# Optimization experiments

Measured on AMD Instinct MI355X. Metric: run time of the kernel, lower is better.

The kernel has to match this reference:

```python
import jax, jax.numpy as jnp
import numpy as np

B, S, HID = 1, 2048, 2048
H = 16
DN, DR, DV = 128, 64, 128          # qk_nope_head_dim, qk_rope_head_dim, v_head_dim
DQ = DN + DR                        # q_head_dim = 192
QLR, KVLR = 1536, 512               # q_lora_rank, kv_lora_rank
MAXP = 32 * 1024
SCALE = DQ ** -0.5
EPS = 1e-6


def rmsnorm(x, w):
    return x * jax.lax.rsqrt(jnp.mean(x * x, axis=-1, keepdims=True) + EPS) * w


def rotate_half(x):
    h = x.shape[-1] // 2
    return jnp.concatenate((-x[..., h:], x[..., :h]), axis=-1)


def interleave_to_half(x):
    # torch: view(b,h,s,d//2,2).transpose(4,3).reshape(b,h,s,d)
    b, h, s, d = x.shape
    return x.reshape(b, h, s, d // 2, 2).transpose(0, 1, 2, 4, 3).reshape(b, h, s, d)


def setup_inputs() -> dict:
    key = jax.random.key(0)
    ks = jax.random.split(key, 8)
    def w(k, shape):
        fan_in = shape[-1]
        return jax.random.normal(k, shape, jnp.float32) * (fan_in ** -0.5)
    inp = {
        "hidden_states": jax.random.normal(ks[0], (B, S, HID), jnp.float32),
        "q_a_w": w(ks[1], (QLR, HID)),
        "q_a_ln": jnp.ones((QLR,), jnp.float32),
        "q_b_w": w(ks[2], (H * DQ, QLR)),
        "kv_a_w": w(ks[3], (KVLR + DR, HID)),
        "kv_a_ln": jnp.ones((KVLR,), jnp.float32),
        "kv_b_w": w(ks[4], (H * (DN + DV), KVLR)),
        "o_w": w(ks[5], (HID, H * DV)),
    }
    # rotary tables, seq_len = 32k
    inv_freq = 1.0 / (10000.0 ** (np.arange(0, DR, 2, dtype=np.float32) / DR))
    t = np.arange(MAXP, dtype=np.float32)
    freqs = np.outer(t, inv_freq)
    emb = np.concatenate((freqs, freqs), axis=-1)
    inp["cos"] = jnp.asarray(np.cos(emb), jnp.float32)
    inp["sin"] = jnp.asarray(np.sin(emb), jnp.float32)
    # bool mask, True = masked (causal)
    inp["attention_mask"] = jnp.triu(jnp.ones((S, S), bool), 1)[None, None]
    inp["position_ids"] = jnp.arange(S, dtype=jnp.int64 if jax.config.jax_enable_x64 else jnp.int32)[None].repeat(B, 0)
    return inp


def reference(hidden_states, q_a_w, q_a_ln, q_b_w, kv_a_w, kv_a_ln, kv_b_w, o_w,
              cos, sin, attention_mask, position_ids):
    b, s, _ = hidden_states.shape
    # low-rank Q: q_b(LN(q_a(x)))
    q = rmsnorm(hidden_states @ q_a_w.T, q_a_ln) @ q_b_w.T         # [b,s,H*DQ]
    q = q.reshape(b, s, H, DQ).transpose(0, 2, 1, 3)               # [b,H,s,DQ]
    q_nope, q_pe = q[..., :DN], q[..., DN:]
    # compressed KV + decoupled rope key
    ckv = hidden_states @ kv_a_w.T                                  # [b,s,KVLR+DR]
    compressed_kv, k_pe = ckv[..., :KVLR], ckv[..., KVLR:]
    k_pe = k_pe.reshape(b, s, 1, DR).transpose(0, 2, 1, 3)          # [b,1,s,DR]
    kv = rmsnorm(compressed_kv, kv_a_ln) @ kv_b_w.T                 # [b,s,H*(DN+DV)]
    kv = kv.reshape(b, s, H, DN + DV).transpose(0, 2, 1, 3)         # [b,H,s,DN+DV]
    k_nope, value_states = kv[..., :DN], kv[..., DN:]
    # rotary with interleaved->half reorder on the rope slice only
    cos_p = cos[position_ids][:, None]                              # [b,1,s,DR]
    sin_p = sin[position_ids][:, None]
    q_pe = interleave_to_half(q_pe)
    k_pe = interleave_to_half(k_pe)
    q_pe = q_pe * cos_p + rotate_half(q_pe) * sin_p
    k_pe = k_pe * cos_p + rotate_half(k_pe) * sin_p
    query_states = jnp.concatenate((q_nope, q_pe), axis=-1)         # [b,H,s,DQ]
    key_states = jnp.concatenate(
        (k_nope, jnp.broadcast_to(k_pe, (b, H, s, DR))), axis=-1)   # [b,H,s,DQ]
    # manual attention
    scores = jnp.einsum("bhqd,bhkd->bhqk", query_states, key_states) * SCALE
    scores = jnp.where(attention_mask, jnp.float32(-10000.0), scores)
    attn = jax.nn.softmax(scores.astype(jnp.float32), axis=-1).astype(query_states.dtype)
    attn_out = jnp.einsum("bhqk,bhkd->bhqd", attn, value_states)    # [b,H,s,DV]
    attn_out = attn_out.transpose(0, 2, 1, 3).reshape(b, s, H * DV)
    return attn_out @ o_w.T                                         # [b,s,HID]
```

## Files before the change

kernel.cpp:

```cpp
#include <hip/hip_runtime.h>
#include <stdint.h>

typedef unsigned short u16;
typedef __attribute__((ext_vector_type(8))) short short8;
typedef __attribute__((ext_vector_type(4))) float f32x4;
typedef __attribute__((ext_vector_type(4))) unsigned short ushort4_t;
typedef __attribute__((ext_vector_type(4))) float float4_t;

#define DEV_INLINE __device__ __forceinline__

DEV_INLINE u16 f2bf(float f) {
    union { float f; unsigned u; } x; x.f = f;
    unsigned u = x.u;
    unsigned r = (u + 0x7FFFu + ((u >> 16) & 1u)) >> 16;
    return (u16)r;
}

DEV_INLINE float bf2f(u16 b) {
    union { unsigned u; float f; } x; x.u = ((unsigned)b) << 16;
    return x.f;
}

DEV_INLINE float fexp2(float x) {
    float r;
    asm("v_exp_f32 %0, %1" : "=v"(r) : "v"(x));
    return r;
}

__global__ void conv_multi(const float* __restrict__ s0, u16* __restrict__ d0, long e0,
                           const float* __restrict__ s1, u16* __restrict__ d1, long e1,
                           const float* __restrict__ s2, u16* __restrict__ d2, long e2,
                           const float* __restrict__ s3, u16* __restrict__ d3, long e3,
                           const float* __restrict__ s4, u16* __restrict__ d4, long e4) {
    long i = (long)blockIdx.x * 256 + threadIdx.x;
    const float* s; u16* d; long base;
    if      (i < e0) { s = s0; d = d0; base = 0; }
    else if (i < e1) { s = s1; d = d1; base = e0; }
    else if (i < e2) { s = s2; d = d2; base = e1; }
    else if (i < e3) { s = s3; d = d3; base = e2; }
    else if (i < e4) { s = s4; d = d4; base = e3; }
    else return;
    long j = i - base;
    float4_t v = ((const float4_t*)s)[j];
    ushort4_t o;
    o.x = f2bf(v.x); o.y = f2bf(v.y); o.z = f2bf(v.z); o.w = f2bf(v.w);
    ((ushort4_t*)d)[j] = o;
}

__global__ void conv_pad(const float* __restrict__ in, u16* __restrict__ out,
                         int rows_valid, long n4, int cols4) {
    long i = (long)blockIdx.x * blockDim.x + threadIdx.x;
    if (i >= n4) return;
    long row = i / cols4;
    ushort4_t o; o.x = 0; o.y = 0; o.z = 0; o.w = 0;
    if (row < rows_valid) {
        float4_t v = ((const float4_t*)in)[i];
        o.x = f2bf(v.x); o.y = f2bf(v.y); o.z = f2bf(v.z); o.w = f2bf(v.w);
    }
    ((ushort4_t*)out)[i] = o;
}

#define BK 32

DEV_INLINE void gload16(const u16* g, u16* l) {
    __builtin_amdgcn_global_load_lds((const __attribute__((address_space(1))) unsigned int*)g,
                                     (__attribute__((address_space(3))) unsigned int*)l,
                                     16, 0, 0);
}

template <typename OT>
__global__ __launch_bounds__(256) void gemm64_db(const u16* __restrict__ A, const u16* __restrict__ B,
                                                 OT* __restrict__ C, int M, int N, int K) {
    __shared__ u16 As[2][64 * BK];
    __shared__ u16 Bs[2][128 * BK];
    const int tid = threadIdx.x;
    const int wid = tid >> 6, lane = tid & 63;
    const int lm = lane & 15, lk = lane >> 4;
    const long bm = (long)blockIdx.y * 64, bn = (long)blockIdx.x * 128;

    f32x4 acc[4][2] = {};

    const int rowS = lane >> 2;
    const int colS = ((lane & 3) ^ ((lane >> 3) & 3)) * 8;
    const int cs = (lm >> 1) & 3;
    const u16* Ag = A + (bm + wid * 16 + rowS) * (long)K + colS;
    const u16* Bg = B + (bn + wid * 32 + rowS) * (long)K + colS;
    const int aoff = wid * 16 * BK;
    const int boff = wid * 32 * BK;

    gload16(Ag, &As[0][aoff]);
    gload16(Bg, &Bs[0][boff]);
    gload16(Bg + 16 * (long)K, &Bs[0][boff + 16 * BK]);
    __syncthreads();

    int cur = 0;
    for (int k0 = 0; k0 < K; k0 += BK) {
        if (k0 + BK < K) {
            gload16(Ag + k0 + BK, &As[cur ^ 1][aoff]);
            gload16(Bg + k0 + BK, &Bs[cur ^ 1][boff]);
            gload16(Bg + 16 * (long)K + k0 + BK, &Bs[cur ^ 1][boff + 16 * BK]);
        }
        short8 af[4], bfr[2];
#pragma unroll
        for (int m = 0; m < 4; ++m)
            af[m] = *(const short8*)&As[cur][(m * 16 + lm) * BK + (lk ^ cs) * 8];
#pragma unroll
        for (int n = 0; n < 2; ++n)
            bfr[n] = *(const short8*)&Bs[cur][(wid * 32 + n * 16 + lm) * BK + (lk ^ cs) * 8];
#pragma unroll
        for (int m = 0; m < 4; ++m)
#pragma unroll
            for (int n = 0; n < 2; ++n)
                acc[m][n] = __builtin_amdgcn_mfma_f32_16x16x32_bf16(af[m], bfr[n], acc[m][n], 0, 0, 0);
        __syncthreads();
        cur ^= 1;
    }

#pragma unroll
    for (int m = 0; m < 4; ++m)
#pragma unroll
        for (int n = 0; n < 2; ++n)
#pragma unroll
            for (int r = 0; r < 4; ++r) {
                long idx = (bm + m * 16 + lk * 4 + r) * (long)N + bn + wid * 32 + n * 16 + lm;
                if constexpr (sizeof(OT) == 4) C[idx] = acc[m][n][r];
                else                           C[idx] = f2bf(acc[m][n][r]);
            }
}

__global__ __launch_bounds__(256) void rmsnorm_bf16(const float* __restrict__ in, const float* __restrict__ w,
                                                    u16* __restrict__ out, int ldin, int ldout, int ncols) {
    const int row = blockIdx.x, tid = threadIdx.x;
    const float* x = in + (long)row * ldin;
    float ss = 0.f;
    for (int c = tid; c < ncols; c += 256) { float v = x[c]; ss = fmaf(v, v, ss); }
#pragma unroll
    for (int off = 32; off > 0; off >>= 1) ss += __shfl_down(ss, off);
    __shared__ float part[4];
    if ((tid & 63) == 0) part[tid >> 6] = ss;
    __syncthreads();
    float tot = part[0] + part[1] + part[2] + part[3];
    float rs = rsqrtf(tot / (float)ncols + 1e-6f);
    for (int c = tid; c < ncols; c += 256) out[(long)row * ldout + c] = f2bf(x[c] * rs * w[c]);
}

__global__ void rope_k(const float* __restrict__ ckv, const int* __restrict__ pos,
                       const float* __restrict__ cosT, const float* __restrict__ sinT,
                       u16* __restrict__ Kb) {
    int idx = blockIdx.x * 256 + threadIdx.x;
    if (idx >= 2048 * 32) return;
    int s = idx >> 5, j = idx & 31;
    long p = pos[s];
    const float* row = ckv + (long)s * 2176 + 2048;
    float x0 = row[2 * j], x1 = row[2 * j + 1];
    float c0 = cosT[p * 64 + j],      s0 = sinT[p * 64 + j];
    float c1 = cosT[p * 64 + 32 + j], s1 = sinT[p * 64 + 32 + j];
    u16 o0 = f2bf(x0 * c0 - x1 * s0);
    u16 o1 = f2bf(x1 * c1 + x0 * s1);
#pragma unroll
    for (int h = 0; h < 16; ++h) {
        u16* kr = Kb + ((long)h * 2048 + s) * 192 + 128;
        kr[j] = o0; kr[32 + j] = o1;
    }
}

__global__ void build_q(const u16* __restrict__ q, const int* __restrict__ pos,
                        const float* __restrict__ cosT, const float* __restrict__ sinT,
                        u16* __restrict__ Qb) {
    long idx = (long)blockIdx.x * 256 + threadIdx.x;
    if (idx >= 16L * 2048 * 192) return;
    int d = (int)(idx % 192);
    int s = (int)((idx / 192) % 2048);
    int h = (int)(idx / (192L * 2048));
    const u16* qrow = q + (long)s * 3072 + h * 192;
    u16 outv;
    if (d < 128) {
        outv = qrow[d];
    } else {
        long p = pos[s];
        int dd = d - 128;
        float cv = cosT[p * 64 + dd], sv = sinT[p * 64 + dd];
        float val;
        if (dd < 32) val = bf2f(qrow[128 + 2 * dd]) * cv - bf2f(qrow[128 + 2 * dd + 1]) * sv;
        else { int jj = dd - 32; val = bf2f(qrow[128 + 2 * jj + 1]) * cv + bf2f(qrow[128 + 2 * jj]) * sv; }
        outv = f2bf(val);
    }
    Qb[((long)h * 2048 + s) * 192 + d] = outv;
}

__global__ __launch_bounds__(256) void build_kv2(const u16* __restrict__ kv, u16* __restrict__ Kb,
                                                 u16* __restrict__ Vt) {
    __shared__ u16 Ls[128][72];
    const int h = blockIdx.y, s0 = blockIdx.x * 64;
    const int tid = threadIdx.x;
#pragma unroll
    for (int i = 0; i < 8; ++i) {
        int u = i * 256 + tid;
        int r = u >> 5, c8 = (u & 31) * 8;
        short8 x = *(const short8*)(kv + (long)(s0 + r) * 4096 + h * 256 + c8);
        if (c8 < 128) {
            *(short8*)(Kb + ((long)h * 2048 + s0 + r) * 192 + c8) = x;
        } else {
#pragma unroll
            for (int j = 0; j < 8; ++j) {
                int d = c8 - 128 + j;
                Ls[d][r ^ (((d >> 3) & 7) << 3)] = (u16)x[j];
            }
        }
    }
    __syncthreads();
#pragma unroll
    for (int i = 0; i < 8; ++i) {
        int u = i * 256 + tid;
        int d = u >> 4, s4 = (u & 15) * 4;
        int swz = ((d >> 3) & 7) << 3;
        ushort4_t v;
        v.x = Ls[d][(s4 + 0) ^ swz]; v.y = Ls[d][(s4 + 1) ^ swz];
        v.z = Ls[d][(s4 + 2) ^ swz]; v.w = Ls[d][(s4 + 3) ^ swz];
        *(ushort4_t*)(Vt + ((long)h * 128 + d) * 2048 + s0 + s4) = v;
    }
}

__global__ __launch_bounds__(512, 2) void attn_fwd(const u16* __restrict__ Qb, const u16* __restrict__ Kb,
                                                   const u16* __restrict__ Vt, u16* __restrict__ Ao) {
    __shared__ __align__(16) char smem[52736];

    const int b = blockIdx.x;
    const int h = (b & 7) * 2 + ((b >> 3) & 1);
    const int pi = b >> 4;
    const int tid = threadIdx.x;
    const int wid = tid >> 6, lane = tid & 63;
    const int lm = lane & 15, lk = lane >> 4;
    const int s = wid >> 2;
    const int wp = wid & 3;
    const int t256 = tid & 255;

    u16* KsS = (u16*)(smem) + s * 6400;
    u16* VsS = (u16*)(smem + 25600) + s * 4096;
    u16* PsW = (u16*)(smem + 41984) + wid * 640;
    float* ML = (float*)(smem + 52224);
    float* Ob = (float*)smem;

    const u16* Kh = Kb + (long)h * 2048 * 192;
    const u16* Vh = Vt + (long)h * 128 * 2048;

    short8 bones = {};
    if (lm == 0) {
#pragma unroll
        for (int j = 0; j < 8; ++j) bones[j] = (short)0x3F80;
    }
    const float C2 = 0.104117548f;

    for (int half = 0; half < 2; ++half) {
        const int qi = half ? (31 - pi) : pi;
        const int q0 = qi * 64;
        const int nt = 2 * qi + 2;
        const int niter = qi + 1;

        short8 qf[6];
        const u16* qbase = Qb + ((long)h * 2048 + q0 + wp * 16 + lm) * 192;
#pragma unroll
        for (int kf = 0; kf < 6; ++kf) qf[kf] = *(const short8*)(qbase + kf * 32 + lk * 8);

        f32x4 o[8] = {};
        f32x4 o9 = {};
        float mrow[4] = {-1e30f, -1e30f, -1e30f, -1e30f};

        short8 kreg[3], vreg[2];
        {
            const long k0 = s * 32;
#pragma unroll
            for (int i = 0; i < 3; ++i) {
                int idx = i * 256 + t256; int r = idx / 24, c = (idx % 24) * 8;
                kreg[i] = *(const short8*)(Kh + (k0 + r) * 192 + c);
            }
#pragma unroll
            for (int i = 0; i < 2; ++i) {
                int idx = i * 256 + t256; int dv = idx >> 2, kvb = idx & 3;
                vreg[i] = *(const short8*)(Vh + (long)dv * 2048 + k0 + kvb * 8);
            }
#pragma unroll
            for (int i = 0; i < 3; ++i) {
                int idx = i * 256 + t256; int r = idx / 24, c = (idx % 24) * 8;
                *(short8*)&KsS[r * 200 + c] = kreg[i];
            }
#pragma unroll
            for (int i = 0; i < 2; ++i) {
                int idx = i * 256 + t256; int dv = idx >> 2, kvb = idx & 3;
                *(short8*)&VsS[kvb * 1024 + ((dv * 8) ^ (kvb * 16))] = vreg[i];
            }
        }
        __syncthreads();

        for (int it = 0; it < niter; ++it) {
            const int ts = 2 * it + s;
            const int k0 = ts * 32;
            const bool more = (it + 1 < niter);

            if (more) {
                const long k0n = (long)(2 * (it + 1) + s) * 32;
#pragma unroll
                for (int i = 0; i < 3; ++i) {
                    int idx = i * 256 + t256; int r = idx / 24, c = (idx % 24) * 8;
                    kreg[i] = *(const short8*)(Kh + (k0n + r) * 192 + c);
                }
#pragma unroll
                for (int i = 0; i < 2; ++i) {
                    int idx = i * 256 + t256; int dv = idx >> 2, kvb = idx & 3;
                    vreg[i] = *(const short8*)(Vh + (long)dv * 2048 + k0n + kvb * 8);
                }
            }

            f32x4 sfr[2] = {};
            __builtin_amdgcn_s_setprio(1);
#pragma unroll
            for (int n = 0; n < 2; ++n)
#pragma unroll
                for (int kf = 0; kf < 6; ++kf) {
                    short8 kb = *(const short8*)&KsS[(n * 16 + lm) * 200 + kf * 32 + lk * 8];
                    sfr[n] = __builtin_amdgcn_mfma_f32_16x16x32_bf16(qf[kf], kb, sfr[n], 0, 0, 0);
                }
            __builtin_amdgcn_s_setprio(0);

            float sv[2][4];
            const bool bt = (ts >= nt - 2);
#pragma unroll
            for (int n = 0; n < 2; ++n)
#pragma unroll
                for (int r = 0; r < 4; ++r) {
                    float val = sfr[n][r] * C2;
                    if (bt && (k0 + n * 16 + lm > q0 + wp * 16 + lk * 4 + r)) val = -1e30f;
                    sv[n][r] = val;
                }

            float pmax[4];
#pragma unroll
            for (int r = 0; r < 4; ++r) {
                float mx = fmaxf(sv[0][r], sv[1][r]);
#pragma unroll
                for (int off = 1; off < 16; off <<= 1) mx = fmaxf(mx, __shfl_xor(mx, off));
                pmax[r] = mx;
            }
            bool need = (pmax[0] > mrow[0] + 8.f) || (pmax[1] > mrow[1] + 8.f) ||
                        (pmax[2] > mrow[2] + 8.f) || (pmax[3] > mrow[3] + 8.f);
            if (__any(need)) {
#pragma unroll
                for (int r = 0; r < 4; ++r) {
                    float mnew = fmaxf(mrow[r], pmax[r]);
                    float alpha = fexp2(mrow[r] - mnew);
                    mrow[r] = mnew;
#pragma unroll
                    for (int d = 0; d < 8; ++d) o[d][r] *= alpha;
                    o9[r] *= alpha;
                }
            }
#pragma unroll
            for (int n = 0; n < 2; ++n)
#pragma unroll
                for (int r = 0; r < 4; ++r)
                    PsW[(lk * 4 + r) * 40 + ((n * 16 + lm) ^ (lk << 3))] = f2bf(fexp2(sv[n][r] - mrow[r]));

            short8 pf = *(const short8*)&PsW[lm * 40 + ((lk ^ ((lm >> 2) & 3)) << 3)];
            __builtin_amdgcn_s_setprio(1);
#pragma unroll
            for (int d = 0; d < 8; ++d) {
                short8 vf = *(const short8*)&VsS[lk * 1024 + (((d * 16 + lm) * 8) ^ (lk * 16))];
                o[d] = __builtin_amdgcn_mfma_f32_16x16x32_bf16(pf, vf, o[d], 0, 0, 0);
            }
            o9 = __builtin_amdgcn_mfma_f32_16x16x32_bf16(pf, bones, o9, 0, 0, 0);
            __builtin_amdgcn_s_setprio(0);

            if (more) {
                __syncthreads();
#pragma unroll
                for (int i = 0; i < 3; ++i) {
                    int idx = i * 256 + t256; int r = idx / 24, c = (idx % 24) * 8;
                    *(short8*)&KsS[r * 200 + c] = kreg[i];
                }
#pragma unroll
                for (int i = 0; i < 2; ++i) {
                    int idx = i * 256 + t256; int dv = idx >> 2, kvb = idx & 3;
                    *(short8*)&VsS[kvb * 1024 + ((dv * 8) ^ (kvb * 16))] = vreg[i];
                }
                __syncthreads();
            }
        }

        __syncthreads();
        if (s == 1) {
#pragma unroll
            for (int d = 0; d < 8; ++d)
#pragma unroll
                for (int r = 0; r < 4; ++r)
                    Ob[(wp * 16 + lk * 4 + r) * 128 + d * 16 + lm] = o[d][r];
            if (lm == 0) {
#pragma unroll
                for (int r = 0; r < 4; ++r) {
                    ML[(wp * 16 + lk * 4 + r) * 2 + 0] = mrow[r];
                    ML[(wp * 16 + lk * 4 + r) * 2 + 1] = o9[r];
                }
            }
        }
        __syncthreads();
        if (s == 0) {
            float e0[4], e1[4], inv[4];
#pragma unroll
            for (int r = 0; r < 4; ++r) {
                float m1 = ML[(wp * 16 + lk * 4 + r) * 2 + 0];
                float l1 = ML[(wp * 16 + lk * 4 + r) * 2 + 1];
                float l0 = __shfl(o9[r], lane & 48);
                float M = fmaxf(mrow[r], m1);
                e0[r] = fexp2(mrow[r] - M);
                e1[r] = fexp2(m1 - M);
                inv[r] = 1.f / (l0 * e0[r] + l1 * e1[r]);
            }
#pragma unroll
            for (int d = 0; d < 8; ++d)
#pragma unroll
                for (int r = 0; r < 4; ++r) {
                    float val = (o[d][r] * e0[r] +
                                 Ob[(wp * 16 + lk * 4 + r) * 128 + d * 16 + lm] * e1[r]) * inv[r];
                    Ao[((long)q0 + wp * 16 + lk * 4 + r) * 2048 + h * 128 + d * 16 + lm] = f2bf(val);
                }
        }
        __syncthreads();
    }
}

extern "C" void kernel_launch(void* const* d_in, const int* in_sizes, int n_in,
                              void* d_out, int out_size, void* d_ws, size_t ws_size,
                              hipStream_t stream) {
    (void)in_sizes; (void)n_in; (void)out_size; (void)ws_size;
    const float* hidden  = (const float*)d_in[0];
    const float* q_a_w   = (const float*)d_in[1];
    const float* q_a_ln  = (const float*)d_in[2];
    const float* q_b_w   = (const float*)d_in[3];
    const float* kv_a_w  = (const float*)d_in[4];
    const float* kv_a_ln = (const float*)d_in[5];
    const float* kv_b_w  = (const float*)d_in[6];
    const float* o_w     = (const float*)d_in[7];
    const float* cosT    = (const float*)d_in[8];
    const float* sinT    = (const float*)d_in[9];
    const int*   pos     = (const int*)d_in[11];

    char* ws = (char*)d_ws;
    u16* o_w_bf   = (u16*)(ws + 0);
    u16* qb_w_bf  = (u16*)(ws + 8388608);
    u16* kvb_w_bf = (u16*)(ws + 17825792);
    u16* qn_bf    = (u16*)(ws + 22020096);
    u16* kvn_bf   = (u16*)(ws + 28311552);
    u16* Qb       = (u16*)(ws + 30408704);
    u16* Kb       = (u16*)(ws + 42991616);
    u16* Vt       = (u16*)(ws + 55574528);
    u16* aout_bf  = (u16*)(ws + 63963136);
    u16*   hid_bf    = (u16*)(ws + 72351744);
    u16*   qkva_w_bf = (u16*)(ws + 80740352);
    float* qkva_f    = (float*)(ws + 89653248);
    u16*   q_f_bf    = (u16*)(ws + 72351744);
    u16*   kv_f_bf   = (u16*)(ws + 89653248);

    conv_multi<<<17920, 256, 0, stream>>>(
        hidden, hid_bf,               1048576L,
        q_a_w,  qkva_w_bf,            1835008L,
        q_b_w,  qb_w_bf,              3014656L,
        kv_b_w, kvb_w_bf,             3538944L,
        o_w,    o_w_bf,               4587520L);
    conv_pad<<<(640L*2048/4 + 255)/256, 256, 0, stream>>>(kv_a_w, qkva_w_bf + 1536L*2048, 576, 640L*2048/4, 512);

    gemm64_db<float><<<dim3(17, 32), 256, 0, stream>>>(hid_bf, qkva_w_bf, qkva_f, 2048, 2176, 2048);

    rmsnorm_bf16<<<2048, 256, 0, stream>>>(qkva_f, q_a_ln, qn_bf, 2176, 1536, 1536);
    rmsnorm_bf16<<<2048, 256, 0, stream>>>(qkva_f + 1536, kv_a_ln, kvn_bf, 2176, 512, 512);
    rope_k<<<(2048*32)/256, 256, 0, stream>>>(qkva_f, pos, cosT, sinT, Kb);

    gemm64_db<u16><<<dim3(24, 32), 256, 0, stream>>>(qn_bf, qb_w_bf, q_f_bf, 2048, 3072, 1536);
    gemm64_db<u16><<<dim3(32, 32), 256, 0, stream>>>(kvn_bf, kvb_w_bf, kv_f_bf, 2048, 4096, 512);

    build_q<<<(unsigned)((16L*2048*192 + 255)/256), 256, 0, stream>>>(q_f_bf, pos, cosT, sinT, Qb);
    build_kv2<<<dim3(32, 16), 256, 0, stream>>>(kv_f_bf, Kb, Vt);

    attn_fwd<<<256, 512, 0, stream>>>(Qb, Kb, Vt, aout_bf);

    gemm64_db<float><<<dim3(16, 32), 256, 0, stream>>>(aout_bf, o_w_bf, (float*)d_out, 2048, 2048, 2048);
}
```

Measured before the change: 255.8 us.

## Double-buffer K/V tiles in attention and use DPP reductions with packed bf16 converts

The attention kernel now keeps two LDS buffers for K and V. The next tile is written into the idle buffer while the current one is consumed, so each loop iteration needs one barrier instead of two. The row-max reduction uses DPP lane permutes instead of shuffles. The probabilities are converted with packed bf16 convert instructions, and the XOR swizzle on the P scratch buffer is dropped. The s_setprio hints are removed as well. Shared memory grows to about 94KB, which allows at most one block per CU (no issue with 256 blocks), and the unswizzled P layout may bring back LDS bank conflicts.

```diff
diff --git a/kernel.cpp b/kernel.cpp
--- a/kernel.cpp
+++ b/kernel.cpp
@@ -25,6 +25,28 @@
     float r;
     asm("v_exp_f32 %0, %1" : "=v"(r) : "v"(x));
     return r;
+}
+
+DEV_INLINE unsigned cvtpk_bf16(float lo, float hi) {
+    unsigned r;
+    asm("v_cvt_pk_bf16_f32 %0, %1, %2" : "=v"(r) : "v"(lo), "v"(hi));
+    return r;
+}
+
+template <int CTRL>
+DEV_INLINE float dppmax(float x) {
+    union { float f; int i; } u; u.f = x;
+    int y = __builtin_amdgcn_update_dpp(u.i, u.i, CTRL, 0xf, 0xf, true);
+    union { int i; float f; } v; v.i = y;
+    return fmaxf(x, v.f);
+}
+
+DEV_INLINE float rmax16(float x) {
+    x = dppmax<0xB1>(x);
+    x = dppmax<0x4E>(x);
+    x = dppmax<0x141>(x);
+    x = dppmax<0x140>(x);
+    return x;
 }
 
 __global__ void conv_multi(const float* __restrict__ s0, u16* __restrict__ d0, long e0,
@@ -221,9 +243,9 @@
     }
 }
 
-__global__ __launch_bounds__(512, 2) void attn_fwd(const u16* __restrict__ Qb, const u16* __restrict__ Kb,
-                                                   const u16* __restrict__ Vt, u16* __restrict__ Ao) {
-    __shared__ __align__(16) char smem[52736];
+__global__ __launch_bounds__(512) void attn_fwd(const u16* __restrict__ Qb, const u16* __restrict__ Kb,
+                                                const u16* __restrict__ Vt, u16* __restrict__ Ao) {
+    __shared__ __align__(16) char smem[94720];
 
     const int b = blockIdx.x;
     const int h = (b & 7) * 2 + ((b >> 3) & 1);
@@ -231,14 +253,13 @@
     const int tid = threadIdx.x;
     const int wid = tid >> 6, lane = tid & 63;
     const int lm = lane & 15, lk = lane >> 4;
-    const int s = wid >> 2;
-    const int wp = wid & 3;
+    const int s = wid >> 2, wp = wid & 3;
     const int t256 = tid & 255;
 
-    u16* KsS = (u16*)(smem) + s * 6400;
-    u16* VsS = (u16*)(smem + 25600) + s * 4096;
-    u16* PsW = (u16*)(smem + 41984) + wid * 640;
-    float* ML = (float*)(smem + 52224);
+    u16* Ks0 = (u16*)smem + s * 12800;
+    u16* Vs0 = (u16*)(smem + 51200) + s * 8192;
+    u16* PsW = (u16*)(smem + 83968) + wid * 640;
+    float* ML = (float*)(smem + 94208);
     float* Ob = (float*)smem;
 
     const u16* Kh = Kb + (long)h * 2048 * 192;
@@ -282,23 +303,24 @@
 #pragma unroll
             for (int i = 0; i < 3; ++i) {
                 int idx = i * 256 + t256; int r = idx / 24, c = (idx % 24) * 8;
-                *(short8*)&KsS[r * 200 + c] = kreg[i];
+                *(short8*)&Ks0[r * 200 + c] = kreg[i];
             }
 #pragma unroll
             for (int i = 0; i < 2; ++i) {
                 int idx = i * 256 + t256; int dv = idx >> 2, kvb = idx & 3;
-                *(short8*)&VsS[kvb * 1024 + ((dv * 8) ^ (kvb * 16))] = vreg[i];
+                *(short8*)&Vs0[kvb * 1024 + ((dv * 8) ^ (kvb * 16))] = vreg[i];
             }
         }
         __syncthreads();
 
+        int cur = 0;
         for (int it = 0; it < niter; ++it) {
             const int ts = 2 * it + s;
             const int k0 = ts * 32;
             const bool more = (it + 1 < niter);
 
             if (more) {
-                const long k0n = (long)(2 * (it + 1) + s) * 32;
+                const long k0n = (long)(ts + 2) * 32;
 #pragma unroll
                 for (int i = 0; i < 3; ++i) {
                     int idx = i * 256 + t256; int r = idx / 24, c = (idx % 24) * 8;
@@ -311,16 +333,17 @@
                 }
             }
 
+            const u16* KsC = Ks0 + cur * 6400;
+            const u16* VsC = Vs0 + cur * 4096;
+
             f32x4 sfr[2] = {};
-            __builtin_amdgcn_s_setprio(1);
 #pragma unroll
             for (int n = 0; n < 2; ++n)
 #pragma unroll
                 for (int kf = 0; kf < 6; ++kf) {
-                    short8 kb = *(const short8*)&KsS[(n * 16 + lm) * 200 + kf * 32 + lk * 8];
+                    short8 kb = *(const short8*)&KsC[(n * 16 + lm) * 200 + kf * 32 + lk * 8];
                     sfr[n] = __builtin_amdgcn_mfma_f32_16x16x32_bf16(qf[kf], kb, sfr[n], 0, 0, 0);
                 }
-            __builtin_amdgcn_s_setprio(0);
 
             float sv[2][4];
             const bool bt = (ts >= nt - 2);
@@ -335,12 +358,8 @@
 
             float pmax[4];
 #pragma unroll
-            for (int r = 0; r < 4; ++r) {
-                float mx = fmaxf(sv[0][r], sv[1][r]);
-#pragma unroll
-                for (int off = 1; off < 16; off <<= 1) mx = fmaxf(mx, __shfl_xor(mx, off));
-                pmax[r] = mx;
-            }
+            for (int r = 0; r < 4; ++r)
+                pmax[r] = rmax16(fmaxf(sv[0][r], sv[1][r]));
             bool need = (pmax[0] > mrow[0] + 8.f) || (pmax[1] > mrow[1] + 8.f) ||
                         (pmax[2] > mrow[2] + 8.f) || (pmax[3] > mrow[3] + 8.f);
             if (__any(need)) {
@@ -355,38 +374,46 @@
                 }
             }
 #pragma unroll
-            for (int n = 0; n < 2; ++n)
-#pragma unroll
-                for (int r = 0; r < 4; ++r)
-                    PsW[(lk * 4 + r) * 40 + ((n * 16 + lm) ^ (lk << 3))] = f2bf(fexp2(sv[n][r] - mrow[r]));
-
-            short8 pf = *(const short8*)&PsW[lm * 40 + ((lk ^ ((lm >> 2) & 3)) << 3)];
-            __builtin_amdgcn_s_setprio(1);
+            for (int n = 0; n < 2; ++n) {
+                float p0 = fexp2(sv[n][0] - mrow[0]);
+                float p1 = fexp2(sv[n][1] - mrow[1]);
+                float p2 = fexp2(sv[n][2] - mrow[2]);
+                float p3 = fexp2(sv[n][3] - mrow[3]);
+                unsigned pk01 = cvtpk_bf16(p0, p1);
+                unsigned pk23 = cvtpk_bf16(p2, p3);
+                int rb = (lk * 4) * 40 + n * 16 + lm;
+                PsW[rb]       = (u16)pk01;
+                PsW[rb + 40]  = (u16)(pk01 >> 16);
+                PsW[rb + 80]  = (u16)pk23;
+                PsW[rb + 120] = (u16)(pk23 >> 16);
+            }
+
+            short8 pf = *(const short8*)&PsW[lm * 40 + lk * 8];
 #pragma unroll
             for (int d = 0; d < 8; ++d) {
-                short8 vf = *(const short8*)&VsS[lk * 1024 + (((d * 16 + lm) * 8) ^ (lk * 16))];
+                short8 vf = *(const short8*)&VsC[lk * 1024 + (((d * 16 + lm) * 8) ^ (lk * 16))];
                 o[d] = __builtin_amdgcn_mfma_f32_16x16x32_bf16(pf, vf, o[d], 0, 0, 0);
             }
             o9 = __builtin_amdgcn_mfma_f32_16x16x32_bf16(pf, bones, o9, 0, 0, 0);
-            __builtin_amdgcn_s_setprio(0);
 
             if (more) {
-                __syncthreads();
+                u16* KsN = Ks0 + (cur ^ 1) * 6400;
+                u16* VsN = Vs0 + (cur ^ 1) * 4096;
 #pragma unroll
                 for (int i = 0; i < 3; ++i) {
                     int idx = i * 256 + t256; int r = idx / 24, c = (idx % 24) * 8;
-                    *(short8*)&KsS[r * 200 + c] = kreg[i];
+                    *(short8*)&KsN[r * 200 + c] = kreg[i];
                 }
 #pragma unroll
                 for (int i = 0; i < 2; ++i) {
                     int idx = i * 256 + t256; int dv = idx >> 2, kvb = idx & 3;
-                    *(short8*)&VsS[kvb * 1024 + ((dv * 8) ^ (kvb * 16))] = vreg[i];
-                }
-                __syncthreads();
-            }
+                    *(short8*)&VsN[kvb * 1024 + ((dv * 8) ^ (kvb * 16))] = vreg[i];
+                }
+            }
+            __syncthreads();
+            cur ^= 1;
         }
 
-        __syncthreads();
         if (s == 1) {
 #pragma unroll
             for (int d = 0; d < 8; ++d)
@@ -396,31 +423,34 @@
             if (lm == 0) {
 #pragma unroll
                 for (int r = 0; r < 4; ++r) {
-                    ML[(wp * 16 + lk * 4 + r) * 2 + 0] = mrow[r];
-                    ML[(wp * 16 + lk * 4 + r) * 2 + 1] = o9[r];
+                    int row = wp * 16 + lk * 4 + r;
+                    ML[row * 2 + 0] = mrow[r];
+                    ML[row * 2 + 1] = o9[r];
                 }
             }
         }
         __syncthreads();
         if (s == 0) {
-            float e0[4], e1[4], inv[4];
+            float e0[4], e1[4], invl[4];
 #pragma unroll
             for (int r = 0; r < 4; ++r) {
-                float m1 = ML[(wp * 16 + lk * 4 + r) * 2 + 0];
-                float l1 = ML[(wp * 16 + lk * 4 + r) * 2 + 1];
+                int row = wp * 16 + lk * 4 + r;
+                float m1 = ML[row * 2 + 0];
+                float l1 = ML[row * 2 + 1];
                 float l0 = __shfl(o9[r], lane & 48);
                 float M = fmaxf(mrow[r], m1);
                 e0[r] = fexp2(mrow[r] - M);
                 e1[r] = fexp2(m1 - M);
-                inv[r] = 1.f / (l0 * e0[r] + l1 * e1[r]);
+                invl[r] = 1.f / (l0 * e0[r] + l1 * e1[r]);
             }
 #pragma unroll
             for (int d = 0; d < 8; ++d)
 #pragma unroll
                 for (int r = 0; r < 4; ++r) {
+                    int row = wp * 16 + lk * 4 + r;
                     float val = (o[d][r] * e0[r] +
-                                 Ob[(wp * 16 + lk * 4 + r) * 128 + d * 16 + lm] * e1[r]) * inv[r];
-                    Ao[((long)q0 + wp * 16 + lk * 4 + r) * 2048 + h * 128 + d * 16 + lm] = f2bf(val);
+                                 Ob[row * 128 + d * 16 + lm] * e1[r]) * invl[r];
+                    Ao[((long)q0 + row) * 2048 + h * 128 + d * 16 + lm] = f2bf(val);
                 }
         }
         __syncthreads();
@@ -460,11 +490,11 @@
     u16*   kv_f_bf   = (u16*)(ws + 89653248);
 
     conv_multi<<<17920, 256, 0, stream>>>(
-        hidden, hid_bf,               1048576L,
-        q_a_w,  qkva_w_bf,            1835008L,
-        q_b_w,  qb_w_bf,              3014656L,
-        kv_b_w, kvb_w_bf,             3538944L,
-        o_w,    o_w_bf,               4587520L);
+        hidden, hid_bf,    1048576L,
+        q_a_w,  qkva_w_bf, 1835008L,
+        q_b_w,  qb_w_bf,   3014656L,
+        kv_b_w, kvb_w_bf,  3538944L,
+        o_w,    o_w_bf,    4587520L);
     conv_pad<<<(640L*2048/4 + 255)/256, 256, 0, stream>>>(kv_a_w, qkva_w_bf + 1536L*2048, 576, 640L*2048/4, 512);
 
     gemm64_db<float><<<dim3(17, 32), 256, 0, stream>>>(hid_bf, qkva_w_bf, qkva_f, 2048, 2176, 2048);
```

New measurement: 246.2 us. 1.04x faster.
